# Optimization experiments

Hardware: AMD Instinct MI355X
Metric: run time of the kernel (lower is better)

## Reference

```python
import jax, jax.numpy as jnp
import numpy as np

N, E, G = 30000, 240000, 1000
F, H = 78, 10            # in-features, GAT heads
HID = F * H              # 780
NEG_SLOPE = 0.2


def setup_inputs() -> dict:
    key = jax.random.key(0)
    ks = jax.random.split(key, 12)
    x = jax.random.normal(ks[0], (N, F), dtype=jnp.float32)
    edge_index = jax.random.randint(ks[1], (2, E), 0, N, dtype=jnp.int32)
    batch = jnp.sort(jax.random.randint(ks[2], (N,), 0, G, dtype=jnp.int32))
    def lin(k, fan_in, shape):
        return (jax.random.normal(k, shape, dtype=jnp.float32)
                / jnp.sqrt(jnp.float32(fan_in)))
    return {
        "x": x,
        "edge_index": edge_index,
        "batch": batch,
        "W_gat": lin(ks[3], F, (F, HID)),          # GATConv lin weight
        "att_src": lin(ks[4], F, (H, F)),          # GAT attention vectors
        "att_dst": lin(ks[5], F, (H, F)),
        "b_gat": jnp.zeros((HID,), jnp.float32),
        "W_gcn": lin(ks[6], HID, (HID, HID)),
        "b_gcn": jnp.zeros((HID,), jnp.float32),
        "W1": lin(ks[7], 2 * HID, (2 * HID, 1500)),
        "b1": jnp.zeros((1500,), jnp.float32),
        "W2": lin(ks[8], 1500, (1500, 128)),
        "b2": jnp.zeros((128,), jnp.float32),
    }


def _with_self_loops(edge_index):
    loop = jnp.arange(N, dtype=edge_index.dtype)
    src = jnp.concatenate([edge_index[0], loop])
    dst = jnp.concatenate([edge_index[1], loop])
    return src, dst


def reference(x, edge_index, batch, W_gat, att_src, att_dst, b_gat,
              W_gcn, b_gcn, W1, b1, W2, b2):
    src, dst = _with_self_loops(edge_index)  # [E+N]

    # ---- GATConv(78 -> 78, heads=10, concat) ----
    h = (x @ W_gat).reshape(N, H, F)                       # [N,H,F]
    a_src = jnp.einsum('nhf,hf->nh', h, att_src)           # [N,H]
    a_dst = jnp.einsum('nhf,hf->nh', h, att_dst)
    e = jax.nn.leaky_relu(a_src[src] + a_dst[dst], NEG_SLOPE)  # [Et,H]
    # segment softmax over incoming edges of each dst node
    e_max = jax.ops.segment_max(e, dst, num_segments=N)
    e_exp = jnp.exp(e - e_max[dst])
    denom = jax.ops.segment_sum(e_exp, dst, num_segments=N)
    alpha = e_exp / denom[dst]                             # [Et,H]
    msg = h[src] * alpha[:, :, None]                       # [Et,H,F]
    out = jax.ops.segment_sum(msg, dst, num_segments=N).reshape(N, HID) + b_gat
    out = jax.nn.relu(out)

    # ---- GCNConv(780 -> 780), symmetric norm with self loops ----
    h2 = out @ W_gcn                                       # [N,HID]
    deg = jax.ops.segment_sum(jnp.ones_like(dst, jnp.float32), dst,
                              num_segments=N)
    dinv = jax.lax.rsqrt(jnp.maximum(deg, 1.0))
    norm = dinv[src] * dinv[dst]                           # [Et]
    out2 = jax.ops.segment_sum(norm[:, None] * h2[src], dst,
                               num_segments=N) + b_gcn
    out2 = jax.nn.relu(out2)

    # ---- global mean / max pool over molecules ----
    counts = jax.ops.segment_sum(jnp.ones((N,), jnp.float32), batch,
                                 num_segments=G)
    gsum = jax.ops.segment_sum(out2, batch, num_segments=G)
    gmean = gsum / jnp.maximum(counts, 1.0)[:, None]
    gmax = jax.ops.segment_max(out2, batch, num_segments=G)
    gmax = jnp.where(counts[:, None] > 0, gmax, 0.0)
    pooled = jnp.concatenate([gmean, gmax], axis=1)        # [G, 1560]

    # ---- MLP head (dropout = identity at eval) ----
    hidfc = jax.nn.relu(pooled @ W1 + b1)
    return hidfc @ W2 + b2                                 # [G, 128]
```

## Files before the change

### kernel.cpp

```cpp
#include <hip/hip_runtime.h>

#define NN 30000
#define EE 240000
#define ET 270000
#define GG 1000
#define NH 10
#define FF 78
#define HID 780
#define NEG_SLOPE 0.2f

#define LD_H 784
#define KP_GCN 832
#define NP_HID 896
#define KP_X 96
#define MP_N 30080
#define KP_P 1600
#define NP_W1 1536
#define LD_FC 1536
#define MP_G 1024

#define MT 128
#define NT 128
#define NBLK 30

#define C_X   (MP_N * KP_X)
#define C_WG  (NP_HID * KP_X)
#define C_WC  (NP_HID * KP_GCN)
#define C_W1  (NP_W1 * KP_P)
#define C_W2  (128 * LD_FC)
#define C_WS  (FF * 2 * NH)
#define C_IN  NN
#define C_TOT (C_X + C_WG + C_WC + C_W1 + C_W2 + C_WS + C_IN)

typedef __bf16 bf16_8 __attribute__((ext_vector_type(8)));
typedef float f32x4 __attribute__((ext_vector_type(4)));

__device__ __forceinline__ void async_copy16(const void* g, void* l) {
  __builtin_amdgcn_global_load_lds(
      (const __attribute__((address_space(1))) void*)g,
      (__attribute__((address_space(3))) void*)l, 16, 0, 0);
}

__device__ __forceinline__ float bf2f(unsigned int bits) {
  return __uint_as_float(bits << 16);
}

template <bool OUT_BF, int KBC>
__global__ __launch_bounds__(256) void mfma_gemm(
    const __bf16* __restrict__ A, const __bf16* __restrict__ BT,
    float* __restrict__ Cf, __bf16* __restrict__ Cb,
    const float* __restrict__ bias, int M, int Kp, int Nout, int ldc,
    int relu, int rp, int nct, int mtiles) {
  constexpr int NCH = KBC / 8;
  constexpr int TST = KBC / 16;
  constexpr int NST = KBC / 32;
  constexpr int STAGE = 2 * NCH * MT * 8 * 2;
  constexpr int SMEM = (STAGE > 32768) ? STAGE : 32768;
  __shared__ char smem[SMEM];
  __bf16 (*As)[MT][8] = (__bf16 (*)[MT][8])smem;
  __bf16 (*Bs)[MT][8] = (__bf16 (*)[MT][8])(smem + (size_t)NCH * MT * 8 * 2);
  int rt, ct;
  if (rp > 0) {
    int bid = blockIdx.x;
    int p = bid & 7, s = bid >> 3;
    int q = s / nct;
    rt = p * rp + q;
    ct = s - q * nct;
    if (rt >= mtiles) return;
  } else {
    rt = blockIdx.y; ct = blockIdx.x;
  }
  int row0 = rt * MT, col0 = ct * NT;
  int tid = threadIdx.x;
  int lane = tid & 63, wave = tid >> 6;
  int wm = (wave & 1) * 64, wn = (wave >> 1) * 64;
  int l15 = lane & 15, quad = lane >> 4;
  f32x4 acc[4][4] = {};

  for (int k0 = 0; k0 < Kp; k0 += KBC) {
    for (int t = 0; t < TST; t++) {
      int base = t * 256 + wave * 64;
      int s = base + lane;
      int kc = s >> 7, r = s & 127;
      const __bf16* g = A + (size_t)(row0 + r) * Kp + k0 + kc * 8;
      async_copy16(g, (char*)&As[0][0][0] + (size_t)base * 16);
    }
    for (int t = 0; t < TST; t++) {
      int base = t * 256 + wave * 64;
      int s = base + lane;
      int kc = s >> 7, r = s & 127;
      const __bf16* g = BT + (size_t)(col0 + r) * Kp + k0 + kc * 8;
      async_copy16(g, (char*)&Bs[0][0][0] + (size_t)base * 16);
    }
    __syncthreads();

    for (int st = 0; st < NST; st++) {
      bf16_8 af[4], bfv[4];
      for (int mt = 0; mt < 4; mt++)
        af[mt] = *(const bf16_8*)&As[st * 4 + quad][wm + mt * 16 + l15][0];
      for (int nt = 0; nt < 4; nt++)
        bfv[nt] = *(const bf16_8*)&Bs[st * 4 + quad][wn + nt * 16 + l15][0];
      for (int mt = 0; mt < 4; mt++)
        for (int nt = 0; nt < 4; nt++)
          acc[mt][nt] = __builtin_amdgcn_mfma_f32_16x16x32_bf16(
              af[mt], bfv[nt], acc[mt][nt], 0, 0, 0);
    }
    __syncthreads();
  }

  if (OUT_BF) {
    __bf16* Cs = (__bf16*)smem;
    for (int nt = 0; nt < 4; nt++) {
      int col_l = wn + nt * 16 + l15;
      int gcol = col0 + col_l;
      bool valid = gcol < Nout;
      float bv = (valid && bias) ? bias[gcol] : 0.f;
      int ch = col_l >> 3, wi = col_l & 7;
      for (int mt = 0; mt < 4; mt++) {
        for (int r = 0; r < 4; r++) {
          int rl = wm + mt * 16 + quad * 4 + r;
          float v = 0.f;
          if (valid) {
            v = acc[mt][nt][r] + bv;
            if (relu) v = fmaxf(v, 0.f);
          }
          Cs[rl * 128 + ((ch ^ (rl & 7)) << 3) + wi] = (__bf16)v;
        }
      }
    }
    __syncthreads();
    for (int idx = tid; idx < MT * 16; idx += 256) {
      int rl = idx >> 4, ch = idx & 15;
      int grow = row0 + rl, gcol = col0 + ch * 8;
      if (grow < M && gcol + 8 <= ldc)
        *(bf16_8*)(Cb + (size_t)grow * ldc + gcol) =
            *(const bf16_8*)&Cs[rl * 128 + ((ch ^ (rl & 7)) << 3)];
    }
  } else {
    for (int nt = 0; nt < 4; nt++) {
      int col = col0 + wn + nt * 16 + l15;
      if (col >= ldc) continue;
      bool valid = col < Nout;
      float bv = (valid && bias) ? bias[col] : 0.f;
      for (int mt = 0; mt < 4; mt++) {
        int rbase = row0 + wm + mt * 16 + quad * 4;
        for (int r = 0; r < 4; r++) {
          int row = rbase + r;
          if (row >= M) continue;
          float v = 0.f;
          if (valid) {
            v = acc[mt][nt][r] + bv;
            if (relu) v = fmaxf(v, 0.f);
          }
          Cf[(size_t)row * ldc + col] = v;
        }
      }
    }
  }
}

__global__ __launch_bounds__(256) void prep_kernel(
    const float* __restrict__ x, const float* __restrict__ W_gat,
    const float* __restrict__ att_src, const float* __restrict__ att_dst,
    const float* __restrict__ W_gcn, const float* __restrict__ W1,
    const float* __restrict__ W2, __bf16* __restrict__ x_bf,
    __bf16* __restrict__ WgatT, __bf16* __restrict__ WgcnT,
    __bf16* __restrict__ W1T, __bf16* __restrict__ W2T,
    float* __restrict__ wsd, int* __restrict__ cnt, int* __restrict__ fill,
    int* __restrict__ lo, int* __restrict__ hi) {
  int gid = blockIdx.x * 256 + threadIdx.x;
  if (gid < C_X) {
    int n = gid / KP_X, k = gid - n * KP_X;
    x_bf[gid] = (__bf16)((n < NN && k < FF) ? x[(size_t)n * FF + k] : 0.f);
    return;
  }
  gid -= C_X;
  if (gid < C_WG) {
    int n = gid / KP_X, k = gid - n * KP_X;
    WgatT[gid] = (__bf16)((n < HID && k < FF) ? W_gat[(size_t)k * HID + n] : 0.f);
    return;
  }
  gid -= C_WG;
  if (gid < C_WC) {
    int n = gid / KP_GCN, k = gid - n * KP_GCN;
    WgcnT[gid] = (__bf16)((n < HID && k < HID) ? W_gcn[(size_t)k * HID + n] : 0.f);
    return;
  }
  gid -= C_WC;
  if (gid < C_W1) {
    int n = gid / KP_P, k = gid - n * KP_P;
    W1T[gid] = (__bf16)((n < 1500 && k < 2 * HID) ? W1[(size_t)k * 1500 + n] : 0.f);
    return;
  }
  gid -= C_W1;
  if (gid < C_W2) {
    int n = gid / LD_FC, k = gid - n * LD_FC;
    W2T[gid] = (__bf16)((n < 128 && k < 1500) ? W2[(size_t)k * 128 + n] : 0.f);
    return;
  }
  gid -= C_W2;
  if (gid < C_WS) {
    int k = gid / (2 * NH), c = gid - k * (2 * NH);
    int h = (c < NH) ? c : c - NH;
    const float* att = (c < NH) ? att_src : att_dst;
    float s = 0.f;
    for (int f = 0; f < FF; f++)
      s += W_gat[(size_t)k * HID + h * FF + f] * att[h * FF + f];
    wsd[k * 2 * NH + c] = s;
    return;
  }
  gid -= C_WS;
  if (gid < C_IN) {
    cnt[gid] = 0; fill[gid] = 0;
    if (gid < GG) { lo[gid] = NN; hi[gid] = 0; }
  }
}

__global__ __launch_bounds__(256) void adot_kernel(
    const float* __restrict__ x, const float* __restrict__ wsd,
    float* __restrict__ a_src, float* __restrict__ a_dst) {
  __shared__ float w_s[FF * 2 * NH];
  for (int i = threadIdx.x; i < FF * 2 * NH; i += 256) w_s[i] = wsd[i];
  __syncthreads();
  int gid = blockIdx.x * 256 + threadIdx.x;
  if (gid >= NN * 2 * NH) return;
  int n = gid / (2 * NH), c = gid - n * (2 * NH);
  float s = 0.f;
  for (int k = 0; k < FF; k++) s += x[(size_t)n * FF + k] * w_s[k * 2 * NH + c];
  if (c < NH) a_src[n * NH + c] = s;
  else        a_dst[n * NH + (c - NH)] = s;
}

__device__ __forceinline__ void edge_sd(const int* __restrict__ ei, int t,
                                        int& s, int& d) {
  if (t < EE) { s = ei[t]; d = ei[EE + t]; }
  else        { s = t - EE; d = t - EE; }
}

__global__ void count_kernel(const int* __restrict__ ei,
                             const int* __restrict__ batch,
                             int* __restrict__ cnt, int* __restrict__ lo,
                             int* __restrict__ hi) {
  int t = blockIdx.x * blockDim.x + threadIdx.x;
  if (t < ET) { int s, d; edge_sd(ei, t, s, d); atomicAdd(&cnt[d], 1); }
  if (t < NN) {
    int g = batch[t];
    atomicMin(&lo[g], t);
    atomicMax(&hi[g], t + 1);
  }
}

__global__ __launch_bounds__(1024) void scan1_kernel(
    const int* __restrict__ cnt, int* __restrict__ row_ptr,
    int* __restrict__ partial) {
  __shared__ int buf[1024];
  int i = blockIdx.x * 1024 + threadIdx.x;
  int v = (i < NN) ? cnt[i] : 0;
  buf[threadIdx.x] = v;
  __syncthreads();
  for (int off = 1; off < 1024; off <<= 1) {
    int t = (threadIdx.x >= off) ? buf[threadIdx.x - off] : 0;
    __syncthreads();
    buf[threadIdx.x] += t;
    __syncthreads();
  }
  if (i < NN) row_ptr[i] = buf[threadIdx.x] - v;
  if (threadIdx.x == 1023) partial[blockIdx.x] = buf[1023];
}

__global__ void scan2_kernel(int* __restrict__ partial,
                             int* __restrict__ offs) {
  if (threadIdx.x == 0) {
    int run = 0;
    for (int b = 0; b < NBLK; b++) { offs[b] = run; run += partial[b]; }
  }
}

__global__ void scan3_kernel(int* __restrict__ row_ptr,
                             const int* __restrict__ offs,
                             const int* __restrict__ cnt,
                             float* __restrict__ dinv) {
  int i = blockIdx.x * blockDim.x + threadIdx.x;
  if (i < NN) {
    row_ptr[i] += offs[i >> 10];
    dinv[i] = rsqrtf((float)max(cnt[i], 1));
  }
  if (i == 0) row_ptr[NN] = ET;
}

__global__ void scatter_kernel(const int* __restrict__ ei,
                               const int* __restrict__ row_ptr,
                               int* __restrict__ fill,
                               const float* __restrict__ a_src,
                               const float* __restrict__ a_dst,
                               int* __restrict__ col_src,
                               float* __restrict__ p_csr) {
  int t = blockIdx.x * blockDim.x + threadIdx.x;
  if (t >= ET) return;
  int s, d; edge_sd(ei, t, s, d);
  int pos = row_ptr[d] + atomicAdd(&fill[d], 1);
  col_src[pos] = s;
#pragma unroll
  for (int h = 0; h < NH; h++) {
    float v = a_src[s * NH + h] + a_dst[d * NH + h];
    v = (v > 0.f) ? v : v * NEG_SLOPE;
    p_csr[(size_t)pos * NH + h] = __expf(v);
  }
}

__global__ __launch_bounds__(256) void gat_aggr_kernel(
    const int* __restrict__ row_ptr, const int* __restrict__ col_src,
    const float* __restrict__ p_csr, const __bf16* __restrict__ h_bf,
    const float* __restrict__ b_gat, __bf16* __restrict__ A_bf) {
  int wave = threadIdx.x >> 6;
  int lane = threadIdx.x & 63;
  int d = blockIdx.x * 4 + wave;
  int beg = row_ptr[d], end = row_ptr[d + 1];
  int f0 = 16 * lane;

  if (lane < 49) {
    int h0 = f0 / FF;
    int split = (h0 + 1) * FF - f0;
    if (split > 16) split = 16;
    int h1 = (h0 < NH - 1) ? h0 + 1 : NH - 1;
    float acc[16] = {};
    float sum0 = 0.f, sum1 = 0.f;
    for (int e = beg; e < end; e += 4) {
      int sidx[4]; float pp0[4], pp1[4];
#pragma unroll
      for (int j = 0; j < 4; j++) {
        bool ok = (e + j < end);
        int ee = ok ? e + j : beg;
        sidx[j] = col_src[ee];
        float q0 = p_csr[(size_t)ee * NH + h0];
        float q1 = p_csr[(size_t)ee * NH + h1];
        pp0[j] = ok ? q0 : 0.f;
        pp1[j] = ok ? q1 : 0.f;
      }
      uint4 rr0[4], rr1[4];
#pragma unroll
      for (int j = 0; j < 4; j++) {
        const __bf16* rowp = h_bf + (size_t)sidx[j] * LD_H + f0;
        rr0[j] = *(const uint4*)rowp;
        rr1[j] = *(const uint4*)(rowp + 8);
      }
#pragma unroll
      for (int j = 0; j < 4; j++) {
        sum0 += pp0[j]; sum1 += pp1[j];
        unsigned int w[8] = {rr0[j].x, rr0[j].y, rr0[j].z, rr0[j].w,
                             rr1[j].x, rr1[j].y, rr1[j].z, rr1[j].w};
#pragma unroll
        for (int k = 0; k < 16; k++) {
          unsigned int bits = (k & 1) ? (w[k >> 1] >> 16) : (w[k >> 1] & 0xffffu);
          acc[k] += bf2f(bits) * ((k < split) ? pp0[j] : pp1[j]);
        }
      }
    }
    float inv0 = 1.f / sum0, inv1 = 1.f / sum1;
    bf16_8 o0, o1;
#pragma unroll
    for (int k = 0; k < 16; k++) {
      int f = f0 + k;
      float val = 0.f;
      if (f < HID)
        val = fmaxf(acc[k] * ((k < split) ? inv0 : inv1) + b_gat[f], 0.f);
      if (k < 8) o0[k] = (__bf16)val; else o1[k - 8] = (__bf16)val;
    }
    *(bf16_8*)(A_bf + (size_t)d * KP_GCN + f0) = o0;
    *(bf16_8*)(A_bf + (size_t)d * KP_GCN + f0 + 8) = o1;
  } else if (lane < 52) {
    bf16_8 z = {};
    *(bf16_8*)(A_bf + (size_t)d * KP_GCN + f0) = z;
    *(bf16_8*)(A_bf + (size_t)d * KP_GCN + f0 + 8) = z;
  }
}

__global__ __launch_bounds__(256) void gcn_aggr_kernel(
    const int* __restrict__ row_ptr, const int* __restrict__ col_src,
    const float* __restrict__ dinv, const __bf16* __restrict__ h2,
    const float* __restrict__ b_gcn, __bf16* __restrict__ out2) {
  int wave = threadIdx.x >> 6;
  int lane = threadIdx.x & 63;
  int d = blockIdx.x * 4 + wave;
  int beg = row_ptr[d], end = row_ptr[d + 1];
  if (lane >= 49) return;
  int f0 = 16 * lane;
  float dv = dinv[d];
  float acc[16] = {};
  for (int e = beg; e < end; e += 4) {
    int sidx[4]; float ww[4];
#pragma unroll
    for (int j = 0; j < 4; j++) {
      bool ok = (e + j < end);
      int ee = ok ? e + j : beg;
      int s = col_src[ee];
      sidx[j] = s;
      ww[j] = ok ? dinv[s] * dv : 0.f;
    }
    uint4 rr0[4], rr1[4];
#pragma unroll
    for (int j = 0; j < 4; j++) {
      const __bf16* rowp = h2 + (size_t)sidx[j] * LD_H + f0;
      rr0[j] = *(const uint4*)rowp;
      rr1[j] = *(const uint4*)(rowp + 8);
    }
#pragma unroll
    for (int j = 0; j < 4; j++) {
      unsigned int wb[8] = {rr0[j].x, rr0[j].y, rr0[j].z, rr0[j].w,
                            rr1[j].x, rr1[j].y, rr1[j].z, rr1[j].w};
#pragma unroll
      for (int k = 0; k < 16; k++) {
        unsigned int bits = (k & 1) ? (wb[k >> 1] >> 16) : (wb[k >> 1] & 0xffffu);
        acc[k] += bf2f(bits) * ww[j];
      }
    }
  }
  bf16_8 o0, o1;
#pragma unroll
  for (int k = 0; k < 16; k++) {
    int f = f0 + k;
    float val = (f < HID) ? fmaxf(acc[k] + b_gcn[f], 0.f) : 0.f;
    if (k < 8) o0[k] = (__bf16)val; else o1[k - 8] = (__bf16)val;
  }
  *(bf16_8*)(out2 + (size_t)d * LD_H + f0) = o0;
  *(bf16_8*)(out2 + (size_t)d * LD_H + f0 + 8) = o1;
}

__global__ __launch_bounds__(128) void pool_kernel(
    const __bf16* __restrict__ out2, const int* __restrict__ lo,
    const int* __restrict__ hi, __bf16* __restrict__ pooled) {
  int g = blockIdx.x;
  int l = lo[g], h = hi[g];
  int t = threadIdx.x;
  if (t >= 98) {
    if (t < 103) {
      int base = 1560 + (t - 98) * 8;
      for (int k = 0; k < 8; k++) pooled[(size_t)g * KP_P + base + k] = (__bf16)0.f;
    }
    return;
  }
  int f0 = 8 * t;
  float s[8] = {}, mx[8];
#pragma unroll
  for (int k = 0; k < 8; k++) mx[k] = -1e30f;
  for (int n = l; n < h; n++) {
    uint4 r = *(const uint4*)(out2 + (size_t)n * LD_H + f0);
    unsigned int w[4] = {r.x, r.y, r.z, r.w};
#pragma unroll
    for (int k = 0; k < 8; k++) {
      unsigned int bits = (k & 1) ? (w[k >> 1] >> 16) : (w[k >> 1] & 0xffffu);
      float v = bf2f(bits);
      s[k] += v;
      mx[k] = fmaxf(mx[k], v);
    }
  }
  float invc = (h > l) ? 1.f / (float)(h - l) : 0.f;
#pragma unroll
  for (int k = 0; k < 8; k++) {
    int f = f0 + k;
    if (f >= HID) continue;
    float mean = (h > l) ? s[k] * invc : 0.f;
    float mxx  = (h > l) ? mx[k] : 0.f;
    pooled[(size_t)g * KP_P + f] = (__bf16)mean;
    pooled[(size_t)g * KP_P + HID + f] = (__bf16)mxx;
  }
}

extern "C" void kernel_launch(void* const* d_in, const int* in_sizes, int n_in,
                              void* d_out, int out_size, void* d_ws,
                              size_t ws_size, hipStream_t stream) {
  const float* x        = (const float*)d_in[0];
  const int*   edge_idx = (const int*)d_in[1];
  const int*   batch    = (const int*)d_in[2];
  const float* W_gat    = (const float*)d_in[3];
  const float* att_src  = (const float*)d_in[4];
  const float* att_dst  = (const float*)d_in[5];
  const float* b_gat    = (const float*)d_in[6];
  const float* W_gcn    = (const float*)d_in[7];
  const float* b_gcn    = (const float*)d_in[8];
  const float* W1       = (const float*)d_in[9];
  const float* b1       = (const float*)d_in[10];
  const float* W2       = (const float*)d_in[11];
  const float* b2       = (const float*)d_in[12];
  float* out = (float*)d_out;
  (void)in_sizes; (void)n_in; (void)out_size; (void)ws_size;

  char* ws = (char*)d_ws;
  size_t off = 0;
  auto alloc = [&](size_t bytes) -> void* {
    void* p = ws + off;
    off += (bytes + 255) & ~(size_t)255;
    return p;
  };
  char*  bufR     = (char*)alloc((size_t)MP_N * KP_GCN * 2);
  __bf16* A_bf    = (__bf16*)bufR;
  __bf16* out2b   = (__bf16*)bufR;
  __bf16* h_bf    = (__bf16*)alloc((size_t)MP_N * LD_H * 2);
  __bf16* h2_bf   = (__bf16*)alloc((size_t)MP_N * LD_H * 2);
  __bf16* x_bf    = (__bf16*)alloc((size_t)MP_N * KP_X * 2);
  __bf16* WgatT   = (__bf16*)alloc((size_t)NP_HID * KP_X * 2);
  __bf16* WgcnT   = (__bf16*)alloc((size_t)NP_HID * KP_GCN * 2);
  __bf16* W1T     = (__bf16*)alloc((size_t)NP_W1 * KP_P * 2);
  __bf16* W2T     = (__bf16*)alloc((size_t)128 * LD_FC * 2);
  __bf16* pooled  = (__bf16*)alloc((size_t)MP_G * KP_P * 2);
  __bf16* hidfc   = (__bf16*)alloc((size_t)MP_G * LD_FC * 2);
  float* wsd      = (float*)alloc((size_t)FF * 2 * NH * 4);
  float* a_src_b  = (float*)alloc((size_t)NN * NH * 4);
  float* a_dst_b  = (float*)alloc((size_t)NN * NH * 4);
  float* p_csr    = (float*)alloc((size_t)ET * NH * 4);
  int*   cnt      = (int*)alloc((size_t)NN * 4);
  int*   fill     = (int*)alloc((size_t)NN * 4);
  int*   row_ptr  = (int*)alloc((size_t)(NN + 1) * 4);
  int*   col_src  = (int*)alloc((size_t)ET * 4);
  int*   partial  = (int*)alloc((size_t)NBLK * 4);
  int*   offs     = (int*)alloc((size_t)NBLK * 4);
  int*   lo       = (int*)alloc((size_t)GG * 4);
  int*   hi       = (int*)alloc((size_t)GG * 4);
  float* dinv     = (float*)alloc((size_t)NN * 4);

  prep_kernel<<<(C_TOT + 255) / 256, 256, 0, stream>>>(
      x, W_gat, att_src, att_dst, W_gcn, W1, W2, x_bf, WgatT, WgcnT, W1T, W2T,
      wsd, cnt, fill, lo, hi);

  {
    dim3 grid(NP_HID / NT, MP_N / MT);
    mfma_gemm<true, 32><<<grid, 256, 0, stream>>>(
        x_bf, WgatT, nullptr, h_bf, nullptr, NN, KP_X, HID, LD_H, 0, 0, 0, 0);
  }
  adot_kernel<<<(NN * 2 * NH + 255) / 256, 256, 0, stream>>>(x, wsd, a_src_b,
                                                             a_dst_b);

  count_kernel<<<(ET + 255) / 256, 256, 0, stream>>>(edge_idx, batch, cnt, lo,
                                                     hi);
  scan1_kernel<<<NBLK, 1024, 0, stream>>>(cnt, row_ptr, partial);
  scan2_kernel<<<1, 64, 0, stream>>>(partial, offs);
  scan3_kernel<<<(NN + 255) / 256, 256, 0, stream>>>(row_ptr, offs, cnt, dinv);
  scatter_kernel<<<(ET + 255) / 256, 256, 0, stream>>>(
      edge_idx, row_ptr, fill, a_src_b, a_dst_b, col_src, p_csr);

  gat_aggr_kernel<<<NN / 4, 256, 0, stream>>>(row_ptr, col_src, p_csr, h_bf,
                                              b_gat, A_bf);
  {
    mfma_gemm<true, 32><<<dim3(8 * 30 * 7), 256, 0, stream>>>(
        A_bf, WgcnT, nullptr, h2_bf, nullptr, NN, KP_GCN, HID, LD_H, 0,
        30, 7, MP_N / MT);
  }
  gcn_aggr_kernel<<<NN / 4, 256, 0, stream>>>(row_ptr, col_src, dinv, h2_bf,
                                              b_gcn, out2b);

  pool_kernel<<<GG, 128, 0, stream>>>(out2b, lo, hi, pooled);

  {
    dim3 grid(NP_W1 / NT, MP_G / MT);
    mfma_gemm<true, 64><<<grid, 256, 0, stream>>>(
        pooled, W1T, nullptr, hidfc, b1, GG, KP_P, 1500, LD_FC, 1, 0, 0, 0);
  }
  {
    dim3 grid(1, MP_G / MT);
    mfma_gemm<false, 64><<<grid, 256, 0, stream>>>(
        hidfc, W2T, out, nullptr, b2, GG, LD_FC, 128, 128, 0, 0, 0, 0);
  }
}
```

Before: 605.7 us.

## Double-buffer GEMM K loop, fuse count/adot and scan kernels, widen edge batches

Adds a double-buffered LDS path to the MFMA GEMM so the next K tile loads while the current one is computed, and uses it for the GAT and GCN GEMMs. It shrinks the GCN K padding from 832 to 800 and narrows the zero-fill of the padding lanes to match. It fuses the degree/batch counting into the attention-dot kernel and folds the small serial scan into the scan fixup kernel, cutting two launches. The gather loops in both aggregation kernels now batch 8 edges instead of 4 to keep more loads in flight, at the cost of higher register pressure.

```diff
diff --git a/kernel.cpp b/kernel.cpp
--- a/kernel.cpp
+++ b/kernel.cpp
@@ -10,7 +10,7 @@
 #define NEG_SLOPE 0.2f
 
 #define LD_H 784
-#define KP_GCN 832
+#define KP_GCN 800
 #define NP_HID 896
 #define KP_X 96
 #define MP_N 30080
@@ -22,6 +22,7 @@
 #define MT 128
 #define NT 128
 #define NBLK 30
+#define EB 8
 
 #define C_X   (MP_N * KP_X)
 #define C_WG  (NP_HID * KP_X)
@@ -45,20 +46,16 @@
   return __uint_as_float(bits << 16);
 }
 
-template <bool OUT_BF, int KBC>
+template <bool OUT_BF, int KBC, bool DBUF>
 __global__ __launch_bounds__(256) void mfma_gemm(
     const __bf16* __restrict__ A, const __bf16* __restrict__ BT,
     float* __restrict__ Cf, __bf16* __restrict__ Cb,
     const float* __restrict__ bias, int M, int Kp, int Nout, int ldc,
     int relu, int rp, int nct, int mtiles) {
-  constexpr int NCH = KBC / 8;
+  constexpr int NST = KBC / 32;
   constexpr int TST = KBC / 16;
-  constexpr int NST = KBC / 32;
-  constexpr int STAGE = 2 * NCH * MT * 8 * 2;
-  constexpr int SMEM = (STAGE > 32768) ? STAGE : 32768;
-  __shared__ char smem[SMEM];
-  __bf16 (*As)[MT][8] = (__bf16 (*)[MT][8])smem;
-  __bf16 (*Bs)[MT][8] = (__bf16 (*)[MT][8])(smem + (size_t)NCH * MT * 8 * 2);
+  constexpr int STAGEB = (KBC / 8) * MT * 8 * 2;
+  __shared__ char smem[32768];
   int rt, ct;
   if (rp > 0) {
     int bid = blockIdx.x;
@@ -77,35 +74,58 @@
   int l15 = lane & 15, quad = lane >> 4;
   f32x4 acc[4][4] = {};
 
-  for (int k0 = 0; k0 < Kp; k0 += KBC) {
+  auto stage = [&](int k0, int buf) {
+    char* baseA = smem + (DBUF ? buf * 2 * STAGEB : 0);
+    char* baseB = baseA + STAGEB;
     for (int t = 0; t < TST; t++) {
       int base = t * 256 + wave * 64;
       int s = base + lane;
       int kc = s >> 7, r = s & 127;
-      const __bf16* g = A + (size_t)(row0 + r) * Kp + k0 + kc * 8;
-      async_copy16(g, (char*)&As[0][0][0] + (size_t)base * 16);
+      async_copy16(A + (size_t)(row0 + r) * Kp + k0 + kc * 8,
+                   baseA + (size_t)base * 16);
     }
     for (int t = 0; t < TST; t++) {
       int base = t * 256 + wave * 64;
       int s = base + lane;
       int kc = s >> 7, r = s & 127;
-      const __bf16* g = BT + (size_t)(col0 + r) * Kp + k0 + kc * 8;
-      async_copy16(g, (char*)&Bs[0][0][0] + (size_t)base * 16);
-    }
-    __syncthreads();
-
+      async_copy16(BT + (size_t)(col0 + r) * Kp + k0 + kc * 8,
+                   baseB + (size_t)base * 16);
+    }
+  };
+  auto compute = [&](int buf) {
+    char* baseA = smem + (DBUF ? buf * 2 * STAGEB : 0);
+    char* baseB = baseA + STAGEB;
     for (int st = 0; st < NST; st++) {
       bf16_8 af[4], bfv[4];
       for (int mt = 0; mt < 4; mt++)
-        af[mt] = *(const bf16_8*)&As[st * 4 + quad][wm + mt * 16 + l15][0];
+        af[mt] = *(const bf16_8*)(baseA +
+            (size_t)((st * 4 + quad) * MT + wm + mt * 16 + l15) * 16);
       for (int nt = 0; nt < 4; nt++)
-        bfv[nt] = *(const bf16_8*)&Bs[st * 4 + quad][wn + nt * 16 + l15][0];
+        bfv[nt] = *(const bf16_8*)(baseB +
+            (size_t)((st * 4 + quad) * MT + wn + nt * 16 + l15) * 16);
       for (int mt = 0; mt < 4; mt++)
         for (int nt = 0; nt < 4; nt++)
           acc[mt][nt] = __builtin_amdgcn_mfma_f32_16x16x32_bf16(
               af[mt], bfv[nt], acc[mt][nt], 0, 0, 0);
     }
+  };
+
+  if (DBUF) {
+    int niter = Kp / KBC;
+    stage(0, 0);
+    for (int k = 0; k < niter; k++) {
+      __syncthreads();
+      if (k + 1 < niter) stage((k + 1) * KBC, (k + 1) & 1);
+      compute(k & 1);
+    }
     __syncthreads();
+  } else {
+    for (int k0 = 0; k0 < Kp; k0 += KBC) {
+      stage(k0, 0);
+      __syncthreads();
+      compute(0);
+      __syncthreads();
+    }
   }
 
   if (OUT_BF) {
@@ -216,38 +236,33 @@
   }
 }
 
-__global__ __launch_bounds__(256) void adot_kernel(
+__device__ __forceinline__ void edge_sd(const int* __restrict__ ei, int t,
+                                        int& s, int& d) {
+  if (t < EE) { s = ei[t]; d = ei[EE + t]; }
+  else        { s = t - EE; d = t - EE; }
+}
+
+__global__ __launch_bounds__(256) void adot_count_kernel(
     const float* __restrict__ x, const float* __restrict__ wsd,
-    float* __restrict__ a_src, float* __restrict__ a_dst) {
+    float* __restrict__ a_src, float* __restrict__ a_dst,
+    const int* __restrict__ ei, const int* __restrict__ batch,
+    int* __restrict__ cnt, int* __restrict__ lo, int* __restrict__ hi) {
   __shared__ float w_s[FF * 2 * NH];
   for (int i = threadIdx.x; i < FF * 2 * NH; i += 256) w_s[i] = wsd[i];
+  int gid = blockIdx.x * 256 + threadIdx.x;
+  if (gid < ET) { int s, d; edge_sd(ei, gid, s, d); atomicAdd(&cnt[d], 1); }
+  if (gid < NN) {
+    int g = batch[gid];
+    atomicMin(&lo[g], gid);
+    atomicMax(&hi[g], gid + 1);
+  }
   __syncthreads();
-  int gid = blockIdx.x * 256 + threadIdx.x;
   if (gid >= NN * 2 * NH) return;
   int n = gid / (2 * NH), c = gid - n * (2 * NH);
   float s = 0.f;
   for (int k = 0; k < FF; k++) s += x[(size_t)n * FF + k] * w_s[k * 2 * NH + c];
   if (c < NH) a_src[n * NH + c] = s;
   else        a_dst[n * NH + (c - NH)] = s;
-}
-
-__device__ __forceinline__ void edge_sd(const int* __restrict__ ei, int t,
-                                        int& s, int& d) {
-  if (t < EE) { s = ei[t]; d = ei[EE + t]; }
-  else        { s = t - EE; d = t - EE; }
-}
-
-__global__ void count_kernel(const int* __restrict__ ei,
-                             const int* __restrict__ batch,
-                             int* __restrict__ cnt, int* __restrict__ lo,
-                             int* __restrict__ hi) {
-  int t = blockIdx.x * blockDim.x + threadIdx.x;
-  if (t < ET) { int s, d; edge_sd(ei, t, s, d); atomicAdd(&cnt[d], 1); }
-  if (t < NN) {
-    int g = batch[t];
-    atomicMin(&lo[g], t);
-    atomicMax(&hi[g], t + 1);
-  }
 }
 
 __global__ __launch_bounds__(1024) void scan1_kernel(
@@ -268,21 +283,18 @@
   if (threadIdx.x == 1023) partial[blockIdx.x] = buf[1023];
 }
 
-__global__ void scan2_kernel(int* __restrict__ partial,
-                             int* __restrict__ offs) {
+__global__ __launch_bounds__(256) void scan3_kernel(
+    int* __restrict__ row_ptr, const int* __restrict__ partial,
+    const int* __restrict__ cnt, float* __restrict__ dinv) {
+  __shared__ int pre[NBLK];
   if (threadIdx.x == 0) {
     int run = 0;
-    for (int b = 0; b < NBLK; b++) { offs[b] = run; run += partial[b]; }
-  }
-}
-
-__global__ void scan3_kernel(int* __restrict__ row_ptr,
-                             const int* __restrict__ offs,
-                             const int* __restrict__ cnt,
-                             float* __restrict__ dinv) {
-  int i = blockIdx.x * blockDim.x + threadIdx.x;
+    for (int b = 0; b < NBLK; b++) { pre[b] = run; run += partial[b]; }
+  }
+  __syncthreads();
+  int i = blockIdx.x * 256 + threadIdx.x;
   if (i < NN) {
-    row_ptr[i] += offs[i >> 10];
+    row_ptr[i] += pre[i >> 10];
     dinv[i] = rsqrtf((float)max(cnt[i], 1));
   }
   if (i == 0) row_ptr[NN] = ET;
@@ -325,10 +337,10 @@
     int h1 = (h0 < NH - 1) ? h0 + 1 : NH - 1;
     float acc[16] = {};
     float sum0 = 0.f, sum1 = 0.f;
-    for (int e = beg; e < end; e += 4) {
-      int sidx[4]; float pp0[4], pp1[4];
-#pragma unroll
-      for (int j = 0; j < 4; j++) {
+    for (int e = beg; e < end; e += EB) {
+      int sidx[EB]; float pp0[EB], pp1[EB];
+#pragma unroll
+      for (int j = 0; j < EB; j++) {
         bool ok = (e + j < end);
         int ee = ok ? e + j : beg;
         sidx[j] = col_src[ee];
@@ -337,15 +349,15 @@
         pp0[j] = ok ? q0 : 0.f;
         pp1[j] = ok ? q1 : 0.f;
       }
-      uint4 rr0[4], rr1[4];
-#pragma unroll
-      for (int j = 0; j < 4; j++) {
+      uint4 rr0[EB], rr1[EB];
+#pragma unroll
+      for (int j = 0; j < EB; j++) {
         const __bf16* rowp = h_bf + (size_t)sidx[j] * LD_H + f0;
         rr0[j] = *(const uint4*)rowp;
         rr1[j] = *(const uint4*)(rowp + 8);
       }
 #pragma unroll
-      for (int j = 0; j < 4; j++) {
+      for (int j = 0; j < EB; j++) {
         sum0 += pp0[j]; sum1 += pp1[j];
         unsigned int w[8] = {rr0[j].x, rr0[j].y, rr0[j].z, rr0[j].w,
                              rr1[j].x, rr1[j].y, rr1[j].z, rr1[j].w};
@@ -368,7 +380,7 @@
     }
     *(bf16_8*)(A_bf + (size_t)d * KP_GCN + f0) = o0;
     *(bf16_8*)(A_bf + (size_t)d * KP_GCN + f0 + 8) = o1;
-  } else if (lane < 52) {
+  } else if (lane == 49) {
     bf16_8 z = {};
     *(bf16_8*)(A_bf + (size_t)d * KP_GCN + f0) = z;
     *(bf16_8*)(A_bf + (size_t)d * KP_GCN + f0 + 8) = z;
@@ -387,25 +399,25 @@
   int f0 = 16 * lane;
   float dv = dinv[d];
   float acc[16] = {};
-  for (int e = beg; e < end; e += 4) {
-    int sidx[4]; float ww[4];
-#pragma unroll
-    for (int j = 0; j < 4; j++) {
+  for (int e = beg; e < end; e += EB) {
+    int sidx[EB]; float ww[EB];
+#pragma unroll
+    for (int j = 0; j < EB; j++) {
       bool ok = (e + j < end);
       int ee = ok ? e + j : beg;
       int s = col_src[ee];
       sidx[j] = s;
       ww[j] = ok ? dinv[s] * dv : 0.f;
     }
-    uint4 rr0[4], rr1[4];
-#pragma unroll
-    for (int j = 0; j < 4; j++) {
+    uint4 rr0[EB], rr1[EB];
+#pragma unroll
+    for (int j = 0; j < EB; j++) {
       const __bf16* rowp = h2 + (size_t)sidx[j] * LD_H + f0;
       rr0[j] = *(const uint4*)rowp;
       rr1[j] = *(const uint4*)(rowp + 8);
     }
 #pragma unroll
-    for (int j = 0; j < 4; j++) {
+    for (int j = 0; j < EB; j++) {
       unsigned int wb[8] = {rr0[j].x, rr0[j].y, rr0[j].z, rr0[j].w,
                             rr1[j].x, rr1[j].y, rr1[j].z, rr1[j].w};
 #pragma unroll
@@ -513,7 +525,6 @@
   int*   row_ptr  = (int*)alloc((size_t)(NN + 1) * 4);
   int*   col_src  = (int*)alloc((size_t)ET * 4);
   int*   partial  = (int*)alloc((size_t)NBLK * 4);
-  int*   offs     = (int*)alloc((size_t)NBLK * 4);
   int*   lo       = (int*)alloc((size_t)GG * 4);
   int*   hi       = (int*)alloc((size_t)GG * 4);
   float* dinv     = (float*)alloc((size_t)NN * 4);
@@ -524,24 +535,22 @@
 
   {
     dim3 grid(NP_HID / NT, MP_N / MT);
-    mfma_gemm<true, 32><<<grid, 256, 0, stream>>>(
+    mfma_gemm<true, 32, true><<<grid, 256, 0, stream>>>(
         x_bf, WgatT, nullptr, h_bf, nullptr, NN, KP_X, HID, LD_H, 0, 0, 0, 0);
   }
-  adot_kernel<<<(NN * 2 * NH + 255) / 256, 256, 0, stream>>>(x, wsd, a_src_b,
-                                                             a_dst_b);
-
-  count_kernel<<<(ET + 255) / 256, 256, 0, stream>>>(edge_idx, batch, cnt, lo,
-                                                     hi);
+  adot_count_kernel<<<(NN * 2 * NH + 255) / 256, 256, 0, stream>>>(
+      x, wsd, a_src_b, a_dst_b, edge_idx, batch, cnt, lo, hi);
+
   scan1_kernel<<<NBLK, 1024, 0, stream>>>(cnt, row_ptr, partial);
-  scan2_kernel<<<1, 64, 0, stream>>>(partial, offs);
-  scan3_kernel<<<(NN + 255) / 256, 256, 0, stream>>>(row_ptr, offs, cnt, dinv);
+  scan3_kernel<<<(NN + 255) / 256, 256, 0, stream>>>(row_ptr, partial, cnt,
+                                                     dinv);
   scatter_kernel<<<(ET + 255) / 256, 256, 0, stream>>>(
       edge_idx, row_ptr, fill, a_src_b, a_dst_b, col_src, p_csr);
 
   gat_aggr_kernel<<<NN / 4, 256, 0, stream>>>(row_ptr, col_src, p_csr, h_bf,
                                               b_gat, A_bf);
   {
-    mfma_gemm<true, 32><<<dim3(8 * 30 * 7), 256, 0, stream>>>(
+    mfma_gemm<true, 32, true><<<dim3(8 * 30 * 7), 256, 0, stream>>>(
         A_bf, WgcnT, nullptr, h2_bf, nullptr, NN, KP_GCN, HID, LD_H, 0,
         30, 7, MP_N / MT);
   }
@@ -552,12 +561,12 @@
 
   {
     dim3 grid(NP_W1 / NT, MP_G / MT);
-    mfma_gemm<true, 64><<<grid, 256, 0, stream>>>(
+    mfma_gemm<true, 64, false><<<grid, 256, 0, stream>>>(
         pooled, W1T, nullptr, hidfc, b1, GG, KP_P, 1500, LD_FC, 1, 0, 0, 0);
   }
   {
     dim3 grid(1, MP_G / MT);
-    mfma_gemm<false, 64><<<grid, 256, 0, stream>>>(
+    mfma_gemm<false, 64, false><<<grid, 256, 0, stream>>>(
         hidfc, W2T, out, nullptr, b2, GG, LD_FC, 128, 128, 0, 0, 0, 0);
   }
 }
```

After: 618.7 us. 1.02x slower.
